# Performance work log

Hardware: AMD Instinct MI355X
Metric: run time of the kernel (lower is better)

The kernel has to match this reference:

```python
import jax, jax.numpy as jnp
import numpy as np

BN_EPS = 1e-5


def _conv1x1(x, w, b):
    # x: (B, Cin, H, W), w: (Cout, Cin), b: (Cout,)
    return jnp.einsum('bchw,oc->bohw', x, w) + b[None, :, None, None]


def _maxpool2(x):
    b, c, h, w = x.shape
    return x.reshape(b, c, h // 2, 2, w // 2, 2).max(axis=(3, 5))


def setup_inputs() -> dict:
    key = jax.random.key(0)
    ks = jax.random.split(key, 12)
    B, Cc, Cg, H, W = 16, 20, 256, 80, 80
    Ci, Cig = Cc // 2, Cg // 2  # 10, 128
    return {
        'x_c': jax.random.uniform(ks[0], (B, Cc, H, W), jnp.float32),
        'x_1': jax.random.uniform(ks[1], (B, Cg, H, W), jnp.float32),
        'theta_w': jax.random.normal(ks[2], (Ci, Cc), jnp.float32) * 0.1,
        'theta_b': jax.random.normal(ks[3], (Ci,), jnp.float32) * 0.1,
        'phi_w': jax.random.normal(ks[4], (Ci, Cc), jnp.float32) * 0.1,
        'phi_b': jax.random.normal(ks[5], (Ci,), jnp.float32) * 0.1,
        'g_w': jax.random.normal(ks[6], (Cig, Cg), jnp.float32) * 0.05,
        'g_b': jax.random.normal(ks[7], (Cig,), jnp.float32) * 0.05,
        'W_w': jax.random.normal(ks[8], (Cg, Cig), jnp.float32) * 0.05,
        'W_b': jax.random.normal(ks[9], (Cg,), jnp.float32) * 0.05,
        'bn_gamma': jax.random.uniform(ks[10], (Cg,), jnp.float32),
        'bn_beta': jax.random.normal(ks[11], (Cg,), jnp.float32) * 0.1,
    }


def reference(x_c, x_1, theta_w, theta_b, phi_w, phi_b, g_w, g_b, W_w, W_b, bn_gamma, bn_beta):
    B, _, H, W = x_1.shape
    Cig = g_w.shape[0]
    # g path: conv1x1 on x_1 then 2x2 maxpool -> (B, Np, Cig), Np = (H/2)*(W/2)
    g_x = _maxpool2(_conv1x1(x_1, g_w, g_b)).reshape(B, Cig, -1).transpose(0, 2, 1)
    # theta: (B, N, Ci) with N = H*W; phi: (B, Ci, Np)
    theta_x = _conv1x1(x_c, theta_w, theta_b).reshape(B, theta_w.shape[0], -1).transpose(0, 2, 1)
    phi_x = _maxpool2(_conv1x1(x_c, phi_w, phi_b)).reshape(B, phi_w.shape[0], -1)
    f = jnp.einsum('bnc,bcm->bnm', theta_x, phi_x)  # (B, 6400, 1600)
    attn = jax.nn.softmax(f, axis=-1)
    y = jnp.einsum('bnm,bmc->bnc', attn, g_x)  # (B, N, Cig)
    y = y.transpose(0, 2, 1).reshape(B, Cig, H, W)
    # W: conv1x1 + BatchNorm2d (training mode, biased variance)
    w_y = _conv1x1(y, W_w, W_b)
    mean = w_y.mean(axis=(0, 2, 3))
    var = w_y.var(axis=(0, 2, 3))
    w_y = (w_y - mean[None, :, None, None]) * jax.lax.rsqrt(var + BN_EPS)[None, :, None, None]
    w_y = w_y * bn_gamma[None, :, None, None] + bn_beta[None, :, None, None]
    return w_y + x_1
```

## Files before the change

kernel.cpp:

```cpp
#include <hip/hip_runtime.h>
#include <math.h>

#define BB 16
#define CC 20
#define CI 10
#define CG 256
#define CIG 128
#define HH 80
#define WW 80
#define NN 6400
#define HP 40
#define WPD 40
#define NP 1600
#define CNT (BB*NN)

#define OFF_THETA 0
#define OFF_PHI   (OFF_THETA + BB*CI*NN)
#define OFF_Y     (OFF_PHI + BB*CI*NP)
#define OFF_SUMY  (OFF_Y + BB*NN*CIG)
#define OFF_MYY   (OFF_SUMY + 128)
#define OFF_A     (OFF_MYY + 128*128)
#define OFF_BC    (OFF_A + 256)
#define OFF_GW16  (OFF_BC + 256)
#define OFF_WW16  (OFF_GW16 + CG*CIG/2)
#define OFF_GT    (OFF_WW16 + CG*CIG/2)
#define OFF_PARTS (OFF_GT + BB*CIG*NP/2)

typedef _Float16 f16x8 __attribute__((ext_vector_type(8)));
typedef float f32x4 __attribute__((ext_vector_type(4)));
typedef float f32x16 __attribute__((ext_vector_type(16)));

__global__ void k0_prep(const float* __restrict__ gw,
                        const float* __restrict__ ww,
                        float* __restrict__ ws) {
    int idx = blockIdx.x * 256 + threadIdx.x;
    if (idx < CG * CIG) {
        int co = idx / CG, ci = idx % CG;
        _Float16* gw16 = (_Float16*)(ws + OFF_GW16);
        gw16[(ci >> 5) * (CIG * 32) + co * 32 + (ci & 31)] = (_Float16)gw[idx];
        _Float16* ww16 = (_Float16*)(ws + OFF_WW16);
        ww16[idx] = (_Float16)ww[idx];
    }
}

__global__ __launch_bounds__(256) void k1_theta(const float* __restrict__ xc,
                                                const float* __restrict__ tw,
                                                const float* __restrict__ tb,
                                                float* __restrict__ ws) {
    __shared__ float w[CI * CC];
    __shared__ float bia[CI];
    int t = threadIdx.x;
    if (t < CI * CC) w[t] = tw[t];
    if (t < CI) bia[t] = tb[t];
    __syncthreads();
    int idx = blockIdx.x * 256 + t;
    int b = idx / NN, n = idx % NN;
    float acc[CI];
#pragma unroll
    for (int o = 0; o < CI; o++) acc[o] = bia[o];
#pragma unroll
    for (int c = 0; c < CC; c++) {
        float x = xc[(b * CC + c) * NN + n];
#pragma unroll
        for (int o = 0; o < CI; o++) acc[o] += w[o * CC + c] * x;
    }
#pragma unroll
    for (int o = 0; o < CI; o++) ws[OFF_THETA + (b * CI + o) * NN + n] = acc[o];
}

__global__ __launch_bounds__(256) void k1_phi(const float* __restrict__ xc,
                                              const float* __restrict__ pw,
                                              const float* __restrict__ pb,
                                              float* __restrict__ ws) {
    __shared__ float w[CI * CC];
    __shared__ float bia[CI];
    int t = threadIdx.x;
    if (t < CI * CC) w[t] = pw[t];
    if (t < CI) bia[t] = pb[t];
    __syncthreads();
    int idx = blockIdx.x * 256 + t;
    int b = idx / NP, mp = idx % NP;
    int hp = mp / WPD, wp = mp % WPD;
    float best[CI];
#pragma unroll
    for (int o = 0; o < CI; o++) best[o] = -1e30f;
#pragma unroll
    for (int p = 0; p < 4; p++) {
        int n = (2 * hp + (p >> 1)) * WW + 2 * wp + (p & 1);
        float acc[CI];
#pragma unroll
        for (int o = 0; o < CI; o++) acc[o] = bia[o];
#pragma unroll
        for (int c = 0; c < CC; c++) {
            float x = xc[(b * CC + c) * NN + n];
#pragma unroll
            for (int o = 0; o < CI; o++) acc[o] += w[o * CC + c] * x;
        }
#pragma unroll
        for (int o = 0; o < CI; o++) best[o] = fmaxf(best[o], acc[o]);
    }
#pragma unroll
    for (int o = 0; o < CI; o++) ws[OFF_PHI + (b * CI + o) * NP + mp] = best[o];
}

__global__ __launch_bounds__(256) void k2_convg(const float* __restrict__ x1,
                                                const float* __restrict__ gb,
                                                float* __restrict__ ws) {
    __shared__ _Float16 smem[21760];
    const int t = threadIdx.x;
    const int w = t >> 6, l = t & 63, h = l >> 5, ln = l & 31;
    const int bid = blockIdx.x;
    const int b = bid / 40, nb = bid % 40;
    const int n0 = nb * 160;
    const ushort* gw16 = (const ushort*)(ws + OFF_GW16);
    const float* xsrc = x1 + (size_t)b * CG * NN + n0;

    f32x16 acc[5];
#pragma unroll
    for (int j = 0; j < 5; j++)
#pragma unroll
        for (int r = 0; r < 16; r++) acc[j][r] = 0.f;

    const int bk = t >> 3, bs = t & 7;
    uint4 ar[2];
    float4 br[5];

#define K2_LOAD(kc)                                                              \
    {                                                                            \
        ar[0] = *(const uint4*)(gw16 + (kc) * 4096 + t * 16);                    \
        ar[1] = *(const uint4*)(gw16 + (kc) * 4096 + t * 16 + 8);                \
        const float* xr = xsrc + (size_t)((kc) * 32 + bk) * NN + bs * 20;        \
        br[0] = *(const float4*)(xr);                                            \
        br[1] = *(const float4*)(xr + 4);                                        \
        br[2] = *(const float4*)(xr + 8);                                        \
        br[3] = *(const float4*)(xr + 12);                                       \
        br[4] = *(const float4*)(xr + 16);                                       \
    }
#define K2_WRITE(p)                                                              \
    {                                                                            \
        _Float16* Ap = smem + (p) * 10368;                                       \
        _Float16* Bp = Ap + 4608;                                                \
        _Float16* ad = Ap + (t >> 1) * 36 + (t & 1) * 16;                        \
        *(uint2*)(ad + 0) = make_uint2(ar[0].x, ar[0].y);                        \
        *(uint2*)(ad + 4) = make_uint2(ar[0].z, ar[0].w);                        \
        *(uint2*)(ad + 8) = make_uint2(ar[1].x, ar[1].y);                        \
        *(uint2*)(ad + 12) = make_uint2(ar[1].z, ar[1].w);                       \
        _Float16* bd = Bp + bk;                                                  \
        for (int i = 0; i < 5; i++) {                                            \
            int nbase = bs * 20 + 4 * i;                                         \
            bd[(nbase + 0) * 36] = (_Float16)br[i].x;                            \
            bd[(nbase + 1) * 36] = (_Float16)br[i].y;                            \
            bd[(nbase + 2) * 36] = (_Float16)br[i].z;                            \
            bd[(nbase + 3) * 36] = (_Float16)br[i].w;                            \
        }                                                                        \
    }

    K2_LOAD(0);
    K2_WRITE(0);
    __syncthreads();

    for (int kc = 0; kc < 8; ++kc) {
        if (kc < 7) K2_LOAD(kc + 1);
        {
            const _Float16* Ap = smem + (kc & 1) * 10368;
            const _Float16* Bp = Ap + 4608;
#pragma unroll
            for (int kk = 0; kk < 2; kk++) {
                union { f16x8 v; uint2 q[2]; } a;
                const _Float16* ap = Ap + (w * 32 + ln) * 36 + kk * 16 + 8 * h;
                a.q[0] = *(const uint2*)(ap);
                a.q[1] = *(const uint2*)(ap + 4);
#pragma unroll
                for (int j = 0; j < 5; j++) {
                    union { f16x8 v; uint2 q[2]; } bb;
                    const _Float16* bp = Bp + (j * 32 + ln) * 36 + kk * 16 + 8 * h;
                    bb.q[0] = *(const uint2*)(bp);
                    bb.q[1] = *(const uint2*)(bp + 4);
                    acc[j] = __builtin_amdgcn_mfma_f32_32x32x16_f16(a.v, bb.v, acc[j], 0, 0, 0);
                }
            }
        }
        if (kc < 7) {
            K2_WRITE((kc + 1) & 1);
            __syncthreads();
        }
    }

    __syncthreads();
    _Float16* gl = smem;
#pragma unroll
    for (int j = 0; j < 5; j++)
#pragma unroll
        for (int r = 0; r < 16; r++) {
            int co = w * 32 + (r & 3) + 8 * (r >> 2) + 4 * h;
            gl[co * 168 + j * 32 + ln] = (_Float16)acc[j][r];
        }
    __syncthreads();
    {
        int co = t >> 1, qq = t & 1;
        float bias = gb[co];
        union { _Float16 hv[20]; uint2 u[5]; } ov;
        const _Float16* row = gl + co * 168;
#pragma unroll
        for (int o = 0; o < 20; o++) {
            int wp = qq * 20 + o;
            float a0 = (float)row[2 * wp], a1 = (float)row[2 * wp + 1];
            float a2 = (float)row[80 + 2 * wp], a3 = (float)row[81 + 2 * wp];
            ov.hv[o] = (_Float16)(fmaxf(fmaxf(a0, a1), fmaxf(a2, a3)) + bias);
        }
        _Float16* gT = (_Float16*)(ws + OFF_GT) + (size_t)(b * CIG + co) * NP + nb * 40 + qq * 20;
#pragma unroll
        for (int i = 0; i < 5; i++) *(uint2*)(gT + i * 4) = ov.u[i];
    }
#undef K2_LOAD
#undef K2_WRITE
}

__global__ __launch_bounds__(512) void k3_attn(float* __restrict__ ws) {
    __shared__ _Float16 Pt[128][72];
    __shared__ _Float16 gTl[128][72];
    __shared__ float l_run[128];
    __shared__ float psum[2][128];
    __shared__ float sum_l[128];

    const int t = threadIdx.x;
    const int w = t >> 6, l = t & 63;
    const int h = l >> 5, q32 = l & 31;
    const int bid = blockIdx.x;
    const int b = bid / 50, nt = bid % 50, n0 = nt * 128;
    const float* theta = ws + OFF_THETA;
    const float* phi   = ws + OFF_PHI;
    const _Float16* gT = (const _Float16*)(ws + OFF_GT) + (size_t)b * CIG * NP;
    const f32x16 z16 = {0.f,0.f,0.f,0.f,0.f,0.f,0.f,0.f,0.f,0.f,0.f,0.f,0.f,0.f,0.f,0.f};

    const int kt = w & 1;
    const int qt = w >> 1;
    const int ct = w >> 1;
    const int qp0 = 2 * (w & 1), qp1 = qp0 + 1;

    f16x8 thB;
#pragma unroll
    for (int j = 0; j < 8; j++) {
        int c = 8 * h + j;
        thB[j] = (c < CI) ? (_Float16)theta[(b * CI + c) * NN + n0 + qt * 32 + q32]
                          : (_Float16)0.f;
    }

    f32x16 acc0 = z16, acc1 = z16;
    if (t < 128) { l_run[t] = 0.f; sum_l[t] = 0.f; }
    const int cst = t >> 2, gp = t & 3;

    f16x8 phA;
#pragma unroll
    for (int j = 0; j < 8; j++) {
        int c = 8 * h + j;
        phA[j] = (c < CI) ? (_Float16)phi[(b * CI + c) * NP + kt * 32 + q32]
                          : (_Float16)0.f;
    }
    __syncthreads();

    for (int cc = 0; cc < 25; cc++) {
        const int m0 = cc * 64;
        const _Float16* gsrc = gT + (size_t)cst * NP + m0 + gp * 16;
        uint4 ga0 = *(const uint4*)(gsrc);
        uint4 ga1 = *(const uint4*)(gsrc + 8);

        f32x16 S = __builtin_amdgcn_mfma_f32_32x32x16_f16(phA, thB, z16, 0, 0, 0);

        f16x8 phAn;
        if (cc < 24) {
            const int m1 = m0 + 64;
#pragma unroll
            for (int j = 0; j < 8; j++) {
                int c = 8 * h + j;
                phAn[j] = (c < CI) ? (_Float16)phi[(b * CI + c) * NP + m1 + kt * 32 + q32]
                                   : (_Float16)0.f;
            }
        }

        float ps = 0.f;
#pragma unroll
        for (int G = 0; G < 4; G++) {
            float e0 = __expf(S[4 * G + 0]);
            float e1 = __expf(S[4 * G + 1]);
            float e2 = __expf(S[4 * G + 2]);
            float e3 = __expf(S[4 * G + 3]);
            ps += (e0 + e1) + (e2 + e3);
            union { _Float16 hv[4]; uint2 u; } pk;
            pk.hv[0] = (_Float16)e0; pk.hv[1] = (_Float16)e1;
            pk.hv[2] = (_Float16)e2; pk.hv[3] = (_Float16)e3;
            *(uint2*)&Pt[qt * 32 + q32][kt * 32 + 8 * G + 4 * h] = pk.u;
        }
        ps += __shfl_xor(ps, 32);
        if (l < 32) psum[kt][qt * 32 + l] = ps;

        *(uint4*)&gTl[cst][gp * 16] = ga0;
        *(uint4*)&gTl[cst][gp * 16 + 8] = ga1;
        __syncthreads();

        if (t < 128) l_run[t] += psum[0][t] + psum[1][t];

        __builtin_amdgcn_s_setprio(1);
#pragma unroll
        for (int kk = 0; kk < 4; kk++) {
            f16x8 gA  = *(const f16x8*)&gTl[ct * 32 + q32][kk * 16 + 8 * h];
            f16x8 pB0 = *(const f16x8*)&Pt[qp0 * 32 + q32][kk * 16 + 8 * h];
            f16x8 pB1 = *(const f16x8*)&Pt[qp1 * 32 + q32][kk * 16 + 8 * h];
            acc0 = __builtin_amdgcn_mfma_f32_32x32x16_f16(gA, pB0, acc0, 0, 0, 0);
            acc1 = __builtin_amdgcn_mfma_f32_32x32x16_f16(gA, pB1, acc1, 0, 0, 0);
        }
        __builtin_amdgcn_s_setprio(0);
        __syncthreads();

        phA = phAn;
    }

    const float inv0 = 1.f / l_run[qp0 * 32 + q32];
    const float inv1 = 1.f / l_run[qp1 * 32 + q32];
    float* y = ws + OFF_Y;
    const int nA = n0 + qp0 * 32 + q32;
    const int nB = n0 + qp1 * 32 + q32;
#pragma unroll
    for (int G = 0; G < 4; G++) {
        int c0 = ct * 32 + 8 * G + 4 * h;
        *(float4*)&y[(size_t)(b * NN + nA) * CIG + c0] =
            make_float4(acc0[4 * G + 0] * inv0, acc0[4 * G + 1] * inv0,
                        acc0[4 * G + 2] * inv0, acc0[4 * G + 3] * inv0);
        *(float4*)&y[(size_t)(b * NN + nB) * CIG + c0] =
            make_float4(acc1[4 * G + 0] * inv1, acc1[4 * G + 1] * inv1,
                        acc1[4 * G + 2] * inv1, acc1[4 * G + 3] * inv1);
    }
#pragma unroll
    for (int G = 0; G < 4; G++)
#pragma unroll
        for (int jj = 0; jj < 4; jj++) {
            float v = acc0[4 * G + jj] * inv0 + acc1[4 * G + jj] * inv1;
            v += __shfl_xor(v, 1);
            v += __shfl_xor(v, 2);
            v += __shfl_xor(v, 4);
            v += __shfl_xor(v, 8);
            v += __shfl_xor(v, 16);
            if (q32 == 0) atomicAdd(&sum_l[ct * 32 + 8 * G + 4 * h + jj], v);
        }
    __syncthreads();
    if (t < 128) ws[OFF_PARTS + t * 800 + bid] = sum_l[t];
}

__global__ __launch_bounds__(256) void k3b_reduce(float* __restrict__ ws) {
    __shared__ float red[256];
    const int t = threadIdx.x, co = blockIdx.x;
    const float4* src = (const float4*)(ws + OFF_PARTS + co * 800);
    float s = 0.f;
    for (int i = t; i < 200; i += 256) {
        float4 v = src[i];
        s += (v.x + v.y) + (v.z + v.w);
    }
    red[t] = s;
    __syncthreads();
    for (int off = 128; off > 0; off >>= 1) {
        if (t < off) red[t] += red[t + off];
        __syncthreads();
    }
    if (t == 0) ws[OFF_SUMY + co] = red[0];
}

__global__ __launch_bounds__(512) void k4_stats(float* __restrict__ ws) {
    __shared__ _Float16 ys[64][132];
    __shared__ float ybar_l[128];
    const int t = threadIdx.x;
    const int w = t >> 6, l = t & 63, h = l >> 5, ln = l & 31;
    const int bid = blockIdx.x;
    const float* y = ws + OFF_Y;
    if (t < 128) ybar_l[t] = ws[OFF_SUMY + t] * (1.0f / (float)CNT);
    __syncthreads();

    const int tk = w >> 1;
    const int tl0 = 2 * (w & 1), tl1 = tl0 + 1;

    f32x16 acc0 = {0.f,0.f,0.f,0.f,0.f,0.f,0.f,0.f,0.f,0.f,0.f,0.f,0.f,0.f,0.f,0.f};
    f32x16 acc1 = acc0;

    for (int ch = 0; ch < 10; ch++) {
        const float* ysrc = y + ((size_t)bid * 640 + ch * 64) * CIG;
#pragma unroll
        for (int i = 0; i < 4; i++) {
            int f4 = i * 512 + t;
            int n = f4 >> 5, c4 = (f4 & 31) * 4;
            float4 v = *(const float4*)(ysrc + f4 * 4);
            union { _Float16 hv[4]; uint2 u; } p;
            p.hv[0] = (_Float16)(v.x - ybar_l[c4]);
            p.hv[1] = (_Float16)(v.y - ybar_l[c4 + 1]);
            p.hv[2] = (_Float16)(v.z - ybar_l[c4 + 2]);
            p.hv[3] = (_Float16)(v.w - ybar_l[c4 + 3]);
            *(uint2*)&ys[n][c4] = p.u;
        }
        __syncthreads();
#pragma unroll
        for (int kk = 0; kk < 4; kk++) {
            f16x8 av, bv0, bv1;
#pragma unroll
            for (int j = 0; j < 8; j++) {
                int n = kk * 16 + 8 * h + j;
                av[j]  = ys[n][tk * 32 + ln];
                bv0[j] = ys[n][tl0 * 32 + ln];
                bv1[j] = ys[n][tl1 * 32 + ln];
            }
            acc0 = __builtin_amdgcn_mfma_f32_32x32x16_f16(av, bv0, acc0, 0, 0, 0);
            acc1 = __builtin_amdgcn_mfma_f32_32x32x16_f16(av, bv1, acc1, 0, 0, 0);
        }
        __syncthreads();
    }

    float* Myy = ws + OFF_MYY;
#pragma unroll
    for (int r = 0; r < 16; r++) {
        int k = tk * 32 + (r & 3) + 8 * (r >> 2) + 4 * h;
        atomicAdd(&Myy[k * 128 + tl0 * 32 + ln], acc0[r]);
        atomicAdd(&Myy[k * 128 + tl1 * 32 + ln], acc1[r]);
    }
}

__global__ __launch_bounds__(128) void k5_bnparams(const float* __restrict__ Ww,
                                                   const float* __restrict__ Wb,
                                                   const float* __restrict__ gamma,
                                                   const float* __restrict__ beta,
                                                   float* __restrict__ ws) {
    __shared__ float w[128];
    __shared__ float red[128];
    int t = threadIdx.x;
    int co = blockIdx.x;
    w[t] = Ww[co * CIG + t];
    __syncthreads();
    const float inv_cnt = 1.0f / (float)CNT;

    const float* M = ws + OFF_MYY;
    float tk = 0.f;
#pragma unroll
    for (int l4 = 0; l4 < 32; l4++) {
        float4 m4 = *(const float4*)&M[t * 128 + l4 * 4];
        tk += m4.x * w[l4 * 4] + m4.y * w[l4 * 4 + 1] + m4.z * w[l4 * 4 + 2] + m4.w * w[l4 * 4 + 3];
    }
    red[t] = w[t] * tk;
    __syncthreads();
    for (int off = 64; off > 0; off >>= 1) {
        if (t < off) red[t] += red[t + off];
        __syncthreads();
    }
    if (t == 0) {
        float var = red[0] * inv_cnt;
        float a = gamma[co] * rsqrtf(var + 1e-5f);
        ws[OFF_A + co] = a;
        ws[OFF_BC + co] = beta[co];
    }
}

__global__ __launch_bounds__(256) void k6_final(const float* __restrict__ x1,
                                                float* __restrict__ out,
                                                const float* __restrict__ ws) {
    __shared__ _Float16 k6s[33792];
    __shared__ float ybar_l[128];
    _Float16* Asm = k6s;
    _Float16* Bsm = k6s + 16896;
    const int t = threadIdx.x;
    const int w = t >> 6, l = t & 63, h = l >> 5, ln = l & 31;
    const int bid = blockIdx.x;
    const int b = bid / 100, rr = bid % 100;
    const int nt = rr >> 1, ch = rr & 1;
    const int n0 = nt * 128, co0 = ch * 128;

    if (t < 128) ybar_l[t] = ws[OFF_SUMY + t] * (1.0f / (float)CNT);
    __syncthreads();

    {
        const ushort* wsrc = (const ushort*)(ws + OFF_WW16) + (size_t)co0 * 128;
#pragma unroll
        for (int i = 0; i < 8; i++) {
            int flat = i * 2048 + t * 8;
            uint4 v = *(const uint4*)(wsrc + flat);
            _Float16* dst = Asm + (flat >> 7) * 132 + (flat & 127);
            *(uint2*)(dst) = make_uint2(v.x, v.y);
            *(uint2*)(dst + 4) = make_uint2(v.z, v.w);
        }
    }
    {
        const float* ysrc = ws + OFF_Y + (size_t)(b * NN + n0) * CIG;
#pragma unroll
        for (int i = 0; i < 16; i++) {
            int flat = i * 1024 + t * 4;
            int kcol = flat & 127;
            float4 v = *(const float4*)(ysrc + flat);
            union { _Float16 hv[4]; uint2 u; } p;
            p.hv[0] = (_Float16)(v.x - ybar_l[kcol]);
            p.hv[1] = (_Float16)(v.y - ybar_l[kcol + 1]);
            p.hv[2] = (_Float16)(v.z - ybar_l[kcol + 2]);
            p.hv[3] = (_Float16)(v.w - ybar_l[kcol + 3]);
            *(uint2*)(Bsm + (flat >> 7) * 132 + kcol) = p.u;
        }
    }
    __syncthreads();

    f32x16 acc[4];
#pragma unroll
    for (int j = 0; j < 4; j++)
#pragma unroll
        for (int r = 0; r < 16; r++) acc[j][r] = 0.f;

#pragma unroll
    for (int kk = 0; kk < 8; kk++) {
        union { f16x8 v; uint2 q[2]; } a;
        const _Float16* ap = Asm + (w * 32 + ln) * 132 + kk * 16 + 8 * h;
        a.q[0] = *(const uint2*)(ap);
        a.q[1] = *(const uint2*)(ap + 4);
#pragma unroll
        for (int j = 0; j < 4; j++) {
            union { f16x8 v; uint2 q[2]; } bb;
            const _Float16* bp = Bsm + (j * 32 + ln) * 132 + kk * 16 + 8 * h;
            bb.q[0] = *(const uint2*)(bp);
            bb.q[1] = *(const uint2*)(bp + 4);
            acc[j] = __builtin_amdgcn_mfma_f32_32x32x16_f16(a.v, bb.v, acc[j], 0, 0, 0);
        }
    }

    const float* Av = ws + OFF_A;
    const float* Bc = ws + OFF_BC;
#pragma unroll
    for (int r = 0; r < 16; r++) {
        int cor = co0 + w * 32 + (r & 3) + 8 * (r >> 2) + 4 * h;
        float a = Av[cor], bc = Bc[cor];
        size_t base = (size_t)(b * CG + cor) * NN + n0;
#pragma unroll
        for (int j = 0; j < 4; j++) {
            int n = j * 32 + ln;
            out[base + n] = acc[j][r] * a + bc + x1[base + n];
        }
    }
}

extern "C" void kernel_launch(void* const* d_in, const int* in_sizes, int n_in,
                              void* d_out, int out_size, void* d_ws, size_t ws_size,
                              hipStream_t stream) {
    const float* x_c     = (const float*)d_in[0];
    const float* x_1     = (const float*)d_in[1];
    const float* theta_w = (const float*)d_in[2];
    const float* theta_b = (const float*)d_in[3];
    const float* phi_w   = (const float*)d_in[4];
    const float* phi_b   = (const float*)d_in[5];
    const float* g_w     = (const float*)d_in[6];
    const float* g_b     = (const float*)d_in[7];
    const float* W_w     = (const float*)d_in[8];
    const float* W_b     = (const float*)d_in[9];
    const float* gammap  = (const float*)d_in[10];
    const float* betap   = (const float*)d_in[11];
    float* out = (float*)d_out;
    float* ws  = (float*)d_ws;

    k0_prep<<<128, 256, 0, stream>>>(g_w, W_w, ws);
    k1_theta<<<400, 256, 0, stream>>>(x_c, theta_w, theta_b, ws);
    k1_phi<<<100, 256, 0, stream>>>(x_c, phi_w, phi_b, ws);
    k2_convg<<<640, 256, 0, stream>>>(x_1, g_b, ws);
    hipMemsetAsync(ws + OFF_MYY, 0, (128 * 128) * sizeof(float), stream);
    k3_attn<<<800, 512, 0, stream>>>(ws);
    k3b_reduce<<<128, 256, 0, stream>>>(ws);
    k4_stats<<<160, 512, 0, stream>>>(ws);
    k5_bnparams<<<256, 128, 0, stream>>>(W_w, W_b, gammap, betap, ws);
    k6_final<<<1600, 256, 0, stream>>>(x_1, out, ws);
}
```

Before: 276.8 us.

## Double-buffer P and g tiles in attention kernel to remove one barrier per chunk

The attention kernel's shared P, g and psum tiles get two buffers, and the first chunk is peeled into a prologue. Each iteration now computes scores and exps for the next chunk while running the PV MFMAs on the current one, with one __syncthreads per iteration instead of two. This is meant to overlap exp/score work and global loads with matrix-core work. In exchange it doubles the LDS used for these tiles, which may lower occupancy, and adds register pressure.

```diff
diff --git a/kernel.cpp b/kernel.cpp
--- a/kernel.cpp
+++ b/kernel.cpp
@@ -217,10 +217,10 @@
 }
 
 __global__ __launch_bounds__(512) void k3_attn(float* __restrict__ ws) {
-    __shared__ _Float16 Pt[128][72];
-    __shared__ _Float16 gTl[128][72];
+    __shared__ _Float16 Pt[2][128][72];
+    __shared__ _Float16 gTl[2][128][72];
     __shared__ float l_run[128];
-    __shared__ float psum[2][128];
+    __shared__ float psum[2][2][128];
     __shared__ float sum_l[128];
 
     const int t = threadIdx.x;
@@ -257,27 +257,17 @@
         phA[j] = (c < CI) ? (_Float16)phi[(b * CI + c) * NP + kt * 32 + q32]
                           : (_Float16)0.f;
     }
-    __syncthreads();
-
-    for (int cc = 0; cc < 25; cc++) {
-        const int m0 = cc * 64;
-        const _Float16* gsrc = gT + (size_t)cst * NP + m0 + gp * 16;
+    {
+        const _Float16* gsrc = gT + (size_t)cst * NP + gp * 16;
         uint4 ga0 = *(const uint4*)(gsrc);
         uint4 ga1 = *(const uint4*)(gsrc + 8);
-
         f32x16 S = __builtin_amdgcn_mfma_f32_32x32x16_f16(phA, thB, z16, 0, 0, 0);
-
-        f16x8 phAn;
-        if (cc < 24) {
-            const int m1 = m0 + 64;
-#pragma unroll
-            for (int j = 0; j < 8; j++) {
-                int c = 8 * h + j;
-                phAn[j] = (c < CI) ? (_Float16)phi[(b * CI + c) * NP + m1 + kt * 32 + q32]
-                                   : (_Float16)0.f;
-            }
-        }
-
+#pragma unroll
+        for (int j = 0; j < 8; j++) {
+            int c = 8 * h + j;
+            phA[j] = (c < CI) ? (_Float16)phi[(b * CI + c) * NP + 64 + kt * 32 + q32]
+                              : (_Float16)0.f;
+        }
         float ps = 0.f;
 #pragma unroll
         for (int G = 0; G < 4; G++) {
@@ -289,30 +279,68 @@
             union { _Float16 hv[4]; uint2 u; } pk;
             pk.hv[0] = (_Float16)e0; pk.hv[1] = (_Float16)e1;
             pk.hv[2] = (_Float16)e2; pk.hv[3] = (_Float16)e3;
-            *(uint2*)&Pt[qt * 32 + q32][kt * 32 + 8 * G + 4 * h] = pk.u;
+            *(uint2*)&Pt[0][qt * 32 + q32][kt * 32 + 8 * G + 4 * h] = pk.u;
         }
         ps += __shfl_xor(ps, 32);
-        if (l < 32) psum[kt][qt * 32 + l] = ps;
-
-        *(uint4*)&gTl[cst][gp * 16] = ga0;
-        *(uint4*)&gTl[cst][gp * 16 + 8] = ga1;
-        __syncthreads();
-
-        if (t < 128) l_run[t] += psum[0][t] + psum[1][t];
+        if (l < 32) psum[0][kt][qt * 32 + l] = ps;
+        *(uint4*)&gTl[0][cst][gp * 16] = ga0;
+        *(uint4*)&gTl[0][cst][gp * 16 + 8] = ga1;
+    }
+    __syncthreads();
+
+    for (int cc = 0; cc < 25; cc++) {
+        const int cur = cc & 1, nxt = cur ^ 1;
+
+        if (cc < 24) {
+            const int m1 = (cc + 1) * 64;
+            const _Float16* gsrc = gT + (size_t)cst * NP + m1 + gp * 16;
+            uint4 ga0 = *(const uint4*)(gsrc);
+            uint4 ga1 = *(const uint4*)(gsrc + 8);
+
+            f32x16 S = __builtin_amdgcn_mfma_f32_32x32x16_f16(phA, thB, z16, 0, 0, 0);
+
+            if (cc < 23) {
+                const int m2 = m1 + 64;
+#pragma unroll
+                for (int j = 0; j < 8; j++) {
+                    int c = 8 * h + j;
+                    phA[j] = (c < CI) ? (_Float16)phi[(b * CI + c) * NP + m2 + kt * 32 + q32]
+                                      : (_Float16)0.f;
+                }
+            }
+
+            float ps = 0.f;
+#pragma unroll
+            for (int G = 0; G < 4; G++) {
+                float e0 = __expf(S[4 * G + 0]);
+                float e1 = __expf(S[4 * G + 1]);
+                float e2 = __expf(S[4 * G + 2]);
+                float e3 = __expf(S[4 * G + 3]);
+                ps += (e0 + e1) + (e2 + e3);
+                union { _Float16 hv[4]; uint2 u; } pk;
+                pk.hv[0] = (_Float16)e0; pk.hv[1] = (_Float16)e1;
+                pk.hv[2] = (_Float16)e2; pk.hv[3] = (_Float16)e3;
+                *(uint2*)&Pt[nxt][qt * 32 + q32][kt * 32 + 8 * G + 4 * h] = pk.u;
+            }
+            ps += __shfl_xor(ps, 32);
+            if (l < 32) psum[nxt][kt][qt * 32 + l] = ps;
+            *(uint4*)&gTl[nxt][cst][gp * 16] = ga0;
+            *(uint4*)&gTl[nxt][cst][gp * 16 + 8] = ga1;
+        }
+
+        if (t < 128) l_run[t] += psum[cur][0][t] + psum[cur][1][t];
 
         __builtin_amdgcn_s_setprio(1);
 #pragma unroll
         for (int kk = 0; kk < 4; kk++) {
-            f16x8 gA  = *(const f16x8*)&gTl[ct * 32 + q32][kk * 16 + 8 * h];
-            f16x8 pB0 = *(const f16x8*)&Pt[qp0 * 32 + q32][kk * 16 + 8 * h];
-            f16x8 pB1 = *(const f16x8*)&Pt[qp1 * 32 + q32][kk * 16 + 8 * h];
+            f16x8 gA  = *(const f16x8*)&gTl[cur][ct * 32 + q32][kk * 16 + 8 * h];
+            f16x8 pB0 = *(const f16x8*)&Pt[cur][qp0 * 32 + q32][kk * 16 + 8 * h];
+            f16x8 pB1 = *(const f16x8*)&Pt[cur][qp1 * 32 + q32][kk * 16 + 8 * h];
             acc0 = __builtin_amdgcn_mfma_f32_32x32x16_f16(gA, pB0, acc0, 0, 0, 0);
             acc1 = __builtin_amdgcn_mfma_f32_32x32x16_f16(gA, pB1, acc1, 0, 0, 0);
         }
         __builtin_amdgcn_s_setprio(0);
         __syncthreads();
-
-        phA = phAn;
     }
 
     const float inv0 = 1.f / l_run[qp0 * 32 + q32];
```

After: 275.3 us. About the same (-0.6%).
